# Kernel tuning notes

Hardware: AMD Instinct MI355X
Metric: run time of the kernel (lower is better)

Reference implementation:

```python
import jax, jax.numpy as jnp
import numpy as np

D_MODEL = 1024
N_HEADS = 16
D_FF = 4096
EPS = 1e-5


def setup_inputs() -> dict:
    key = jax.random.key(0)
    ks = jax.random.split(key, 16)
    B, S, D, F = 2, 2048, D_MODEL, D_FF
    s_d = 1.0 / np.sqrt(D)
    s_f = 1.0 / np.sqrt(F)
    return {
        "x": jax.random.normal(ks[0], (B, S, D), dtype=jnp.float32),
        "pad_mask": jnp.ones((B, S), dtype=jnp.int32),
        "ln1_g": jnp.ones((D,), jnp.float32), "ln1_b": jnp.zeros((D,), jnp.float32),
        "ln2_g": jnp.ones((D,), jnp.float32), "ln2_b": jnp.zeros((D,), jnp.float32),
        # weights stored [in, out] (equivalent to torch Linear weight.T)
        "wq": jax.random.normal(ks[1], (D, D), jnp.float32) * s_d,
        "bq": jnp.zeros((D,), jnp.float32),
        "wk": jax.random.normal(ks[2], (D, D), jnp.float32) * s_d,
        "bk": jnp.zeros((D,), jnp.float32),
        "wv": jax.random.normal(ks[3], (D, D), jnp.float32) * s_d,
        "bv": jnp.zeros((D,), jnp.float32),
        "wo": jax.random.normal(ks[4], (D, D), jnp.float32) * s_d,
        "bo": jnp.zeros((D,), jnp.float32),
        "w1": jax.random.normal(ks[5], (D, F), jnp.float32) * s_d,
        "b1": jnp.zeros((F,), jnp.float32),
        "w2": jax.random.normal(ks[6], (F, D), jnp.float32) * s_f,
        "b2": jnp.zeros((D,), jnp.float32),
    }


def _layernorm(x, g, b):
    mu = jnp.mean(x, axis=-1, keepdims=True)
    var = jnp.mean(jnp.square(x - mu), axis=-1, keepdims=True)
    return (x - mu) * jax.lax.rsqrt(var + EPS) * g + b


def reference(x, pad_mask, ln1_g, ln1_b, ln2_g, ln2_b,
              wq, bq, wk, bk, wv, bv, wo, bo, w1, b1, w2, b2):
    B, S, D = x.shape
    H = N_HEADS
    dk = D // H

    # mask: causal [1,1,S,S] * pad [B,1,1,S]
    causal = jnp.tril(jnp.ones((S, S), dtype=jnp.int32))[None, None]
    mask = pad_mask[:, None, None, :] * causal  # [B,1,S,S]

    h = _layernorm(x, ln1_g, ln1_b)
    q = (h @ wq + bq).reshape(B, S, H, dk).transpose(0, 2, 1, 3)
    k = (h @ wk + bk).reshape(B, S, H, dk).transpose(0, 2, 1, 3)
    v = (h @ wv + bv).reshape(B, S, H, dk).transpose(0, 2, 1, 3)

    scores = jnp.einsum('bhqd,bhkd->bhqk', q, k) / np.sqrt(dk)
    scores = jnp.where(mask == 0, -jnp.inf, scores)
    attn = jax.nn.softmax(scores, axis=-1)
    ctx = jnp.einsum('bhqk,bhkd->bhqd', attn, v)
    ctx = ctx.transpose(0, 2, 1, 3).reshape(B, S, D)
    x = x + ctx @ wo + bo

    h2 = _layernorm(x, ln2_g, ln2_b)
    ff = jax.nn.gelu(h2 @ w1 + b1, approximate=False) @ w2 + b2
    return x + ff
```

## Files before the change

kernel.cpp:

```cpp
#include <hip/hip_runtime.h>
#include <math.h>


typedef unsigned short bfu;
typedef unsigned short u16x4 __attribute__((ext_vector_type(4)));
typedef unsigned short u16x8 __attribute__((ext_vector_type(8)));
typedef __bf16         bf16x8 __attribute__((ext_vector_type(8)));
typedef float          f32x4 __attribute__((ext_vector_type(4)));

#define SEQ   2048
#define NTOK  4096
#define DM    1024
#define DKH   64

static __device__ __forceinline__ float bfu2f(bfu u) {
  return __uint_as_float(((unsigned)u) << 16);
}
static __device__ __forceinline__ bfu f2bfu(float f) {
  unsigned u = __float_as_uint(f);
  u += 0x7FFFu + ((u >> 16) & 1u);
  return (bfu)(u >> 16);
}
static __device__ __forceinline__ float ldF(const void* p, size_t i, bool isbf) {
  return isbf ? bfu2f(((const bfu*)p)[i]) : ((const float*)p)[i];
}
static __device__ __forceinline__ bool dt_isbf(const void* dt) {
  return *(const unsigned*)dt == 0x3F803F80u;
}
static __device__ __forceinline__ void g2l16(const void* g, void* l) {
  __builtin_amdgcn_global_load_lds((const __attribute__((address_space(1))) void*)g,
                                   (__attribute__((address_space(3))) void*)l,
                                   16, 0, 0);
}

static __device__ __forceinline__ void tr_tile(const void* in, bfu* out,
                                               int R, int C, int gx, int gy,
                                               bool isbf, bfu t[64][65]) {
  const int tx = threadIdx.x & 63, ty = threadIdx.x >> 6;
#pragma unroll
  for (int i = 0; i < 16; ++i) {
    int rr = i * 4 + ty;
    size_t idx = (size_t)(gy + rr) * C + gx + tx;
    t[rr][tx] = isbf ? ((const bfu*)in)[idx] : f2bfu(((const float*)in)[idx]);
  }
  __syncthreads();
#pragma unroll
  for (int i = 0; i < 16; ++i) {
    int cc = i * 4 + ty;
    out[(size_t)(gx + cc) * R + gy + tx] = t[tx][cc];
  }
}

__global__ __launch_bounds__(256) void prep_k(
    const void* ln1g, const void* ln1b, const void* ln2g, const void* ln2b,
    const void* bq, const void* bk, const void* bv, const void* bo,
    const void* b1, const void* b2,
    const void* wq, const void* wk, const void* wv, const void* wo,
    const void* w1, const void* w2,
    bfu* __restrict__ vecs, bfu* __restrict__ wqkvT, bfu* __restrict__ woT,
    bfu* __restrict__ w1T, bfu* __restrict__ w2T) {
  __shared__ bfu t[64][65];
  const bool isbf = dt_isbf(ln1g);
  const int bid = blockIdx.x, tid = threadIdx.x;
  if (bid < 52) {
    const void* src; int segStart, segDst;
    if      (bid < 4)  { src = ln1g; segStart = 0;  segDst = 0; }
    else if (bid < 8)  { src = ln1b; segStart = 4;  segDst = 1024; }
    else if (bid < 12) { src = ln2g; segStart = 8;  segDst = 2048; }
    else if (bid < 16) { src = ln2b; segStart = 12; segDst = 3072; }
    else if (bid < 20) { src = bq;   segStart = 16; segDst = 4096; }
    else if (bid < 24) { src = bk;   segStart = 20; segDst = 5120; }
    else if (bid < 28) { src = bv;   segStart = 24; segDst = 6144; }
    else if (bid < 32) { src = bo;   segStart = 28; segDst = 7168; }
    else if (bid < 48) { src = b1;   segStart = 32; segDst = 8192; }
    else               { src = b2;   segStart = 48; segDst = 12288; }
    const int off = (bid - segStart) * 256 + tid;
    vecs[segDst + off] = isbf ? ((const bfu*)src)[off]
                              : f2bfu(((const float*)src)[off]);
    return;
  }
  const void* in; bfu* out; int R, C, gx, gy;
  const int j = bid - 52;
  if (j < 1024) {
    const int mat = j >> 8, rem = j & 255;
    in  = (mat == 0) ? wq : (mat == 1) ? wk : (mat == 2) ? wv : wo;
    out = (mat == 0) ? wqkvT : (mat == 1) ? wqkvT + 1048576
        : (mat == 2) ? wqkvT + 2097152 : woT;
    R = 1024; C = 1024; gx = (rem & 15) * 64; gy = (rem >> 4) * 64;
  } else if (j < 2048) {
    const int rem = j - 1024;
    in = w1; out = w1T; R = 1024; C = 4096;
    gx = (rem & 63) * 64; gy = (rem >> 6) * 64;
  } else {
    const int rem = j - 2048;
    in = w2; out = w2T; R = 4096; C = 1024;
    gx = (rem & 15) * 64; gy = (rem >> 4) * 64;
  }
  tr_tile(in, out, R, C, gx, gy, isbf, t);
}

__global__ __launch_bounds__(256) void trw2_k(const void* __restrict__ w2,
                                              bfu* __restrict__ out,
                                              const void* __restrict__ dt) {
  __shared__ bfu t[64][65];
  const bool isbf = dt_isbf(dt);
  const int rem = blockIdx.x;
  tr_tile(w2, out, 4096, 1024, (rem & 15) * 64, (rem >> 4) * 64, isbf, t);
}

template <bool RAW>
__global__ __launch_bounds__(256) void ln_k(const void* __restrict__ xin,
                                            const bfu* __restrict__ g,
                                            const bfu* __restrict__ bb,
                                            bfu* __restrict__ y,
                                            const void* __restrict__ dt) {
  const int t = threadIdx.x;
  const size_t base = (size_t)blockIdx.x * DM;
  const int c0 = t * 4;
  float v[4];
  bool isbf = true;
  if constexpr (RAW) isbf = dt_isbf(dt);
  if (!RAW || isbf) {
    u16x4 u = *(const u16x4*)((const bfu*)xin + base + c0);
#pragma unroll
    for (int i = 0; i < 4; ++i) v[i] = bfu2f(u[i]);
  } else {
    float4 f = *(const float4*)((const float*)xin + base + c0);
    v[0] = f.x; v[1] = f.y; v[2] = f.z; v[3] = f.w;
  }
  float s1 = v[0] + v[1] + v[2] + v[3];
  float s2 = v[0]*v[0] + v[1]*v[1] + v[2]*v[2] + v[3]*v[3];
#pragma unroll
  for (int o = 32; o; o >>= 1) {
    s1 += __shfl_xor(s1, o);
    s2 += __shfl_xor(s2, o);
  }
  __shared__ float r1[4], r2[4];
  const int wid = t >> 6, lane = t & 63;
  if (lane == 0) { r1[wid] = s1; r2[wid] = s2; }
  __syncthreads();
  s1 = r1[0] + r1[1] + r1[2] + r1[3];
  s2 = r2[0] + r2[1] + r2[2] + r2[3];
  const float mu = s1 * (1.0f / DM);
  const float var = s2 * (1.0f / DM) - mu * mu;
  const float rs = rsqrtf(var + 1e-5f);
  u16x4 gv = *(const u16x4*)&g[c0];
  u16x4 bv = *(const u16x4*)&bb[c0];
  u16x4 ov;
#pragma unroll
  for (int i = 0; i < 4; ++i)
    ov[i] = f2bfu((v[i] - mu) * rs * bfu2f(gv[i]) + bfu2f(bv[i]));
  *(u16x4*)&y[base + c0] = ov;
}

template <int EPI, int BM>
__global__ __launch_bounds__(256) void gemm_bt(const bfu* __restrict__ A,
                                               const bfu* __restrict__ Bt,
                                               const bfu* __restrict__ bias,
                                               const void* __restrict__ res,
                                               void* __restrict__ C,
                                               int M, int N, int K,
                                               const void* __restrict__ dt) {
  constexpr int NF = (BM == 128) ? 4 : 2;
  __shared__ __align__(16) bfu Asm[BM * 32];
  __shared__ __align__(16) bfu Bsm[128 * 32];
  const bool isbf = dt_isbf(dt);
  const int tid = threadIdx.x;
  const int m0 = blockIdx.y * BM, n0 = blockIdx.x * 128;
  const int wid = tid >> 6, lane = tid & 63;
  const int wm = (BM == 128) ? (wid >> 1) * 64 : 0;
  const int wn = (BM == 128) ? (wid & 1) * 64 : wid * 32;
  const int quad = lane >> 4, l16 = lane & 15;

  f32x4 acc[4][NF] = {};

  const int c0 = tid, c1 = tid + 256;
  const bfu* agp0 = A + (size_t)(m0 + (c0 >> 2)) * K + (c0 & 3) * 8;
  const bfu* agp1 = A + (size_t)(m0 + ((c1 >> 2) & (BM - 1))) * K + (c1 & 3) * 8;
  const bfu* bgp0 = Bt + (size_t)(n0 + (c0 >> 2)) * K + (c0 & 3) * 8;
  const bfu* bgp1 = Bt + (size_t)(n0 + (c1 >> 2)) * K + (c1 & 3) * 8;
  bfu* al0 = Asm + c0 * 8;
  bfu* al1 = Asm + (BM == 128 ? c1 * 8 : 0);
  bfu* bl0 = Bsm + c0 * 8;
  bfu* bl1 = Bsm + c1 * 8;

  for (int k0 = 0; k0 < K; k0 += 32) {
    g2l16(agp0 + k0, al0);
    if constexpr (BM == 128) g2l16(agp1 + k0, al1);
    g2l16(bgp0 + k0, bl0);
    g2l16(bgp1 + k0, bl1);
    __syncthreads();

    u16x8 af[4], bfr[NF];
#pragma unroll
    for (int i = 0; i < 4; ++i)
      af[i] = *(const u16x8*)&Asm[(wm + i * 16 + l16) * 32 + quad * 8];
#pragma unroll
    for (int i = 0; i < NF; ++i)
      bfr[i] = *(const u16x8*)&Bsm[(wn + i * 16 + l16) * 32 + quad * 8];
#pragma unroll
    for (int mi = 0; mi < 4; ++mi)
#pragma unroll
      for (int ni = 0; ni < NF; ++ni)
        acc[mi][ni] = __builtin_amdgcn_mfma_f32_16x16x32_bf16(
            __builtin_bit_cast(bf16x8, af[mi]),
            __builtin_bit_cast(bf16x8, bfr[ni]), acc[mi][ni], 0, 0, 0);
    __syncthreads();
  }

#pragma unroll
  for (int mi = 0; mi < 4; ++mi) {
#pragma unroll
    for (int ni = 0; ni < NF; ++ni) {
      const int col = n0 + wn + ni * 16 + l16;
      const float bvv = bfu2f(bias[col]);
#pragma unroll
      for (int r = 0; r < 4; ++r) {
        const int row = m0 + wm + mi * 16 + quad * 4 + r;
        const size_t idx = (size_t)row * N + col;
        float v = acc[mi][ni][r] + bvv;
        if constexpr (EPI == 1) {
          v = 0.5f * v * (1.0f + erff(v * 0.70710678118f));
          ((bfu*)C)[idx] = f2bfu(v);
        } else if constexpr (EPI == 2) {
          v += ldF(res, idx, isbf);
          ((bfu*)C)[idx] = f2bfu(v);
        } else if constexpr (EPI == 3) {
          v += bfu2f(((const bfu*)res)[idx]);
          if (isbf) ((bfu*)C)[idx] = f2bfu(v);
          else      ((float*)C)[idx] = v;
        } else {
          ((bfu*)C)[idx] = f2bfu(v);
        }
      }
    }
  }
}

#define NEG_BIG (-1e30f)
#define KSTR 72

__global__ __launch_bounds__(256) void attn_flash(const bfu* __restrict__ qkv,
                                                  const int* __restrict__ pad,
                                                  bfu* __restrict__ ctx) {
  __shared__ __align__(16) bfu Kb[64 * KSTR];
  __shared__ __align__(16) bfu VT[64 * KSTR];
  __shared__ __align__(16) bfu Pb[4][16 * KSTR];

  const int tid = threadIdx.x;
  const int wid = tid >> 6, lane = tid & 63;
  const int quad = lane >> 4, l16 = lane & 15;
  const int bh = blockIdx.x;
  const int b = bh >> 4, h = bh & 15;
  const int yq = blockIdx.y;
  const int qt = (yq < 8) ? yq : (yq < 16) ? 23 - yq
               : (yq < 24) ? yq : 55 - yq;
  const int q0 = qt * 64;

  const bfu* qptr = qkv + (size_t)(b * SEQ + q0 + wid * 16 + l16) * 3072 + h * 64 + quad * 8;
  u16x8 qfr[2];
#pragma unroll
  for (int kt = 0; kt < 2; ++kt) {
    u16x8 qr = *(const u16x8*)(qptr + kt * 32);
#pragma unroll
    for (int j = 0; j < 8; ++j) qr[j] = f2bfu(bfu2f(qr[j]) * 0.125f);
    qfr[kt] = qr;
  }

  f32x4 Ofr[4] = {};
  float mrow[4], lrow[4];
#pragma unroll
  for (int r = 0; r < 4; ++r) { mrow[r] = NEG_BIG; lrow[r] = 0.0f; }

  const bfu* kvbase = qkv + (size_t)(b * SEQ) * 3072 + h * 64;
  const int* pb = pad + b * SEQ;
  const int qrow_base = q0 + wid * 16 + quad * 4;

  const int ntiles = qt + 1;
  for (int t = 0; t < ntiles; ++t) {
    const int k0 = t * 64;
    __syncthreads();

#pragma unroll
    for (int s = 0; s < 2; ++s) {
      const int cc = tid + s * 256;
      const int key = cc >> 3, pc = cc & 7;
      u16x8 kv8 = *(const u16x8*)(kvbase + (size_t)(k0 + key) * 3072 + 1024 + pc * 8);
      *(u16x8*)&Kb[key * KSTR + pc * 8] = kv8;
    }
    {
      const int vkey = tid & 63, dblk = tid >> 6;
      const bfu* vp = kvbase + (size_t)(k0 + vkey) * 3072 + 2048 + dblk * 16;
      u16x8 v0 = *(const u16x8*)vp;
      u16x8 v1 = *(const u16x8*)(vp + 8);
#pragma unroll
      for (int j = 0; j < 8; ++j) VT[(dblk * 16 + j) * KSTR + vkey] = v0[j];
#pragma unroll
      for (int j = 0; j < 8; ++j) VT[(dblk * 16 + 8 + j) * KSTR + vkey] = v1[j];
    }
    __syncthreads();

    f32x4 S[4] = {};
#pragma unroll
    for (int nt = 0; nt < 4; ++nt)
#pragma unroll
      for (int kt = 0; kt < 2; ++kt) {
        u16x8 bf = *(const u16x8*)&Kb[(nt * 16 + l16) * KSTR + kt * 32 + quad * 8];
        S[nt] = __builtin_amdgcn_mfma_f32_16x16x32_bf16(
            __builtin_bit_cast(bf16x8, qfr[kt]),
            __builtin_bit_cast(bf16x8, bf), S[nt], 0, 0, 0);
      }

    const bool edge = (t == qt);
    float p[4][4];
    float cmax[4] = {NEG_BIG, NEG_BIG, NEG_BIG, NEG_BIG};
#pragma unroll
    for (int nt = 0; nt < 4; ++nt) {
      const int key = k0 + nt * 16 + l16;
      const bool ok = (pb[key] != 0);
#pragma unroll
      for (int r = 0; r < 4; ++r) {
        float s = (ok && (!edge || key <= qrow_base + r)) ? S[nt][r] : NEG_BIG;
        p[nt][r] = s;
        cmax[r] = fmaxf(cmax[r], s);
      }
    }
#pragma unroll
    for (int off = 1; off < 16; off <<= 1)
#pragma unroll
      for (int r = 0; r < 4; ++r)
        cmax[r] = fmaxf(cmax[r], __shfl_xor(cmax[r], off));
    float alpha[4];
#pragma unroll
    for (int r = 0; r < 4; ++r) {
      const float mn = fmaxf(mrow[r], cmax[r]);
      alpha[r] = __expf(mrow[r] - mn);
      mrow[r] = mn;
    }
    float psum[4] = {0, 0, 0, 0};
#pragma unroll
    for (int nt = 0; nt < 4; ++nt)
#pragma unroll
      for (int r = 0; r < 4; ++r) {
        p[nt][r] = __expf(p[nt][r] - mrow[r]);
        psum[r] += p[nt][r];
      }
#pragma unroll
    for (int off = 1; off < 16; off <<= 1)
#pragma unroll
      for (int r = 0; r < 4; ++r) psum[r] += __shfl_xor(psum[r], off);
#pragma unroll
    for (int r = 0; r < 4; ++r) lrow[r] = lrow[r] * alpha[r] + psum[r];
#pragma unroll
    for (int n = 0; n < 4; ++n)
#pragma unroll
      for (int r = 0; r < 4; ++r) Ofr[n][r] *= alpha[r];

#pragma unroll
    for (int nt = 0; nt < 4; ++nt)
#pragma unroll
      for (int r = 0; r < 4; ++r)
        Pb[wid][(quad * 4 + r) * KSTR + nt * 16 + l16] = f2bfu(p[nt][r]);

#pragma unroll
    for (int at = 0; at < 2; ++at) {
      u16x8 af = *(const u16x8*)&Pb[wid][l16 * KSTR + at * 32 + quad * 8];
#pragma unroll
      for (int n = 0; n < 4; ++n) {
        u16x8 bf = *(const u16x8*)&VT[(n * 16 + l16) * KSTR + at * 32 + quad * 8];
        Ofr[n] = __builtin_amdgcn_mfma_f32_16x16x32_bf16(
            __builtin_bit_cast(bf16x8, af),
            __builtin_bit_cast(bf16x8, bf), Ofr[n], 0, 0, 0);
      }
    }
  }

  float inv[4];
#pragma unroll
  for (int r = 0; r < 4; ++r) inv[r] = 1.0f / lrow[r];
#pragma unroll
  for (int n = 0; n < 4; ++n)
#pragma unroll
    for (int r = 0; r < 4; ++r)
      ctx[(size_t)(b * SEQ + qrow_base + r) * DM + h * 64 + n * 16 + l16] =
          f2bfu(Ofr[n][r] * inv[r]);
}

extern "C" void kernel_launch(void* const* d_in, const int* in_sizes, int n_in,
                              void* d_out, int out_size, void* d_ws, size_t ws_size,
                              hipStream_t stream) {
  (void)in_sizes; (void)n_in; (void)out_size;
  const void* x    = d_in[0];
  const int*  pad  = (const int*)d_in[1];
  const void* ln1g = d_in[2];
  const void* ln1b = d_in[3];
  const void* ln2g = d_in[4];
  const void* ln2b = d_in[5];
  const void* wq   = d_in[6];
  const void* bq   = d_in[7];
  const void* wk   = d_in[8];
  const void* bk   = d_in[9];
  const void* wv   = d_in[10];
  const void* bv   = d_in[11];
  const void* wo   = d_in[12];
  const void* bo   = d_in[13];
  const void* w1   = d_in[14];
  const void* b1   = d_in[15];
  const void* w2   = d_in[16];
  const void* b2   = d_in[17];

  const bool flat = ws_size >= (size_t)(37765120 + 1024) * 2;
  bfu* base  = (bfu*)d_ws;
  bfu* vecs  = base;
  bfu* wqkvT = vecs  + 16384;
  bfu* woT   = wqkvT + 3145728;
  bfu* w1T   = woT   + 1048576;
  bfu* w2Tf  = w1T   + 4194304;
  bfu* h     = w2Tf  + (flat ? 4194304 : 0);
  bfu* qkv   = h     + 4194304;
  bfu* ctx   = qkv   + 12582912;
  bfu* x1    = ctx   + 4194304;
  bfu* ffh   = qkv;
  bfu* w2T   = flat ? w2Tf : h;

  const dim3 blk(256);
  bfu* lg1 = vecs;        bfu* lb1 = vecs + 1024;
  bfu* lg2 = vecs + 2048; bfu* lb2 = vecs + 3072;
  bfu* bqkv = vecs + 4096;
  bfu* boc  = vecs + 7168;
  bfu* b1c  = vecs + 8192;
  bfu* b2c  = vecs + 12288;

  prep_k<<<dim3(flat ? 3124 : 2100), blk, 0, stream>>>(
      ln1g, ln1b, ln2g, ln2b, bq, bk, bv, bo, b1, b2,
      wq, wk, wv, wo, w1, w2, vecs, wqkvT, woT, w1T, w2T);

  ln_k<true><<<dim3(NTOK), blk, 0, stream>>>(x, lg1, lb1, h, ln1g);
  gemm_bt<0, 128><<<dim3(24, 32), blk, 0, stream>>>(h, wqkvT, bqkv, nullptr,
                                                    qkv, NTOK, 3072, 1024, ln1g);
  attn_flash<<<dim3(32, 32), blk, 0, stream>>>(qkv, pad, ctx);
  gemm_bt<2, 64><<<dim3(8, 64), blk, 0, stream>>>(ctx, woT, boc, x, x1,
                                                  NTOK, 1024, 1024, ln1g);
  ln_k<false><<<dim3(NTOK), blk, 0, stream>>>(x1, lg2, lb2, h, ln1g);
  gemm_bt<1, 128><<<dim3(32, 32), blk, 0, stream>>>(h, w1T, b1c, nullptr, ffh,
                                                    NTOK, 4096, 1024, ln1g);
  if (!flat) trw2_k<<<dim3(1024), blk, 0, stream>>>(w2, w2T, ln1g);
  gemm_bt<3, 64><<<dim3(8, 64), blk, 0, stream>>>(ffh, w2T, b2c, x1, d_out,
                                                  NTOK, 1024, 4096, ln1g);
}
```

Before: 472.0 us.

## Add 32-row GEMM tile variant for N=1024 GEMMs and prefetch K/V tiles in attention

Result: faster. 452.4 us (-4.2%).

```diff
diff --git a/kernel.cpp b/kernel.cpp
--- a/kernel.cpp
+++ b/kernel.cpp
@@ -153,7 +153,7 @@
   *(u16x4*)&y[base + c0] = ov;
 }
 
-template <int EPI, int BM>
+template <int EPI>
 __global__ __launch_bounds__(256) void gemm_bt(const bfu* __restrict__ A,
                                                const bfu* __restrict__ Bt,
                                                const bfu* __restrict__ bias,
@@ -161,47 +161,45 @@
                                                void* __restrict__ C,
                                                int M, int N, int K,
                                                const void* __restrict__ dt) {
-  constexpr int NF = (BM == 128) ? 4 : 2;
-  __shared__ __align__(16) bfu Asm[BM * 32];
+  __shared__ __align__(16) bfu Asm[128 * 32];
   __shared__ __align__(16) bfu Bsm[128 * 32];
   const bool isbf = dt_isbf(dt);
   const int tid = threadIdx.x;
-  const int m0 = blockIdx.y * BM, n0 = blockIdx.x * 128;
+  const int m0 = blockIdx.y * 128, n0 = blockIdx.x * 128;
   const int wid = tid >> 6, lane = tid & 63;
-  const int wm = (BM == 128) ? (wid >> 1) * 64 : 0;
-  const int wn = (BM == 128) ? (wid & 1) * 64 : wid * 32;
+  const int wm = (wid >> 1) * 64, wn = (wid & 1) * 64;
   const int quad = lane >> 4, l16 = lane & 15;
 
-  f32x4 acc[4][NF] = {};
+  f32x4 acc[4][4] = {};
 
   const int c0 = tid, c1 = tid + 256;
   const bfu* agp0 = A + (size_t)(m0 + (c0 >> 2)) * K + (c0 & 3) * 8;
-  const bfu* agp1 = A + (size_t)(m0 + ((c1 >> 2) & (BM - 1))) * K + (c1 & 3) * 8;
+  const bfu* agp1 = A + (size_t)(m0 + (c1 >> 2)) * K + (c1 & 3) * 8;
   const bfu* bgp0 = Bt + (size_t)(n0 + (c0 >> 2)) * K + (c0 & 3) * 8;
   const bfu* bgp1 = Bt + (size_t)(n0 + (c1 >> 2)) * K + (c1 & 3) * 8;
   bfu* al0 = Asm + c0 * 8;
-  bfu* al1 = Asm + (BM == 128 ? c1 * 8 : 0);
+  bfu* al1 = Asm + c1 * 8;
   bfu* bl0 = Bsm + c0 * 8;
   bfu* bl1 = Bsm + c1 * 8;
 
   for (int k0 = 0; k0 < K; k0 += 32) {
     g2l16(agp0 + k0, al0);
-    if constexpr (BM == 128) g2l16(agp1 + k0, al1);
+    g2l16(agp1 + k0, al1);
     g2l16(bgp0 + k0, bl0);
     g2l16(bgp1 + k0, bl1);
     __syncthreads();
 
-    u16x8 af[4], bfr[NF];
+    u16x8 af[4], bfr[4];
 #pragma unroll
     for (int i = 0; i < 4; ++i)
       af[i] = *(const u16x8*)&Asm[(wm + i * 16 + l16) * 32 + quad * 8];
 #pragma unroll
-    for (int i = 0; i < NF; ++i)
+    for (int i = 0; i < 4; ++i)
       bfr[i] = *(const u16x8*)&Bsm[(wn + i * 16 + l16) * 32 + quad * 8];
 #pragma unroll
     for (int mi = 0; mi < 4; ++mi)
 #pragma unroll
-      for (int ni = 0; ni < NF; ++ni)
+      for (int ni = 0; ni < 4; ++ni)
         acc[mi][ni] = __builtin_amdgcn_mfma_f32_16x16x32_bf16(
             __builtin_bit_cast(bf16x8, af[mi]),
             __builtin_bit_cast(bf16x8, bfr[ni]), acc[mi][ni], 0, 0, 0);
@@ -211,7 +209,7 @@
 #pragma unroll
   for (int mi = 0; mi < 4; ++mi) {
 #pragma unroll
-    for (int ni = 0; ni < NF; ++ni) {
+    for (int ni = 0; ni < 4; ++ni) {
       const int col = n0 + wn + ni * 16 + l16;
       const float bvv = bfu2f(bias[col]);
 #pragma unroll
@@ -237,6 +235,94 @@
   }
 }
 
+template <int EPI>
+__global__ __launch_bounds__(256) void gemm32_bt(const bfu* __restrict__ A,
+                                                 const bfu* __restrict__ Bt,
+                                                 const bfu* __restrict__ bias,
+                                                 const void* __restrict__ res,
+                                                 void* __restrict__ C,
+                                                 int M, int N, int K,
+                                                 const void* __restrict__ dt) {
+  __shared__ __align__(16) bfu Asm[2 * 32 * 32];
+  __shared__ __align__(16) bfu Bsm[2 * 128 * 32];
+  const bool isbf = dt_isbf(dt);
+  const int tid = threadIdx.x;
+  const int m0 = blockIdx.y * 32, n0 = blockIdx.x * 128;
+  const int wid = tid >> 6, lane = tid & 63;
+  const int wn = wid * 32;
+  const int quad = lane >> 4, l16 = lane & 15;
+
+  f32x4 acc[2][2] = {};
+
+  const int pA = tid >> 7, rA = (tid >> 2) & 31, qA = tid & 3;
+  const bfu* agp = A + (size_t)(m0 + rA) * K + pA * 32 + qA * 8;
+  bfu* aldst = Asm + tid * 8;
+  const bfu* bgp[4]; bfu* bldst[4];
+#pragma unroll
+  for (int s = 0; s < 4; ++s) {
+    const int c = tid + s * 256;
+    const int pB = c >> 9, rB = (c >> 2) & 127, qB = c & 3;
+    bgp[s] = Bt + (size_t)(n0 + rB) * K + pB * 32 + qB * 8;
+    bldst[s] = Bsm + c * 8;
+  }
+
+  for (int k0 = 0; k0 < K; k0 += 64) {
+    g2l16(agp + k0, aldst);
+#pragma unroll
+    for (int s = 0; s < 4; ++s) g2l16(bgp[s] + k0, bldst[s]);
+    __syncthreads();
+
+    u16x8 af[2][2], bfr[2][2];
+#pragma unroll
+    for (int kt = 0; kt < 2; ++kt) {
+#pragma unroll
+      for (int mi = 0; mi < 2; ++mi)
+        af[mi][kt] = *(const u16x8*)&Asm[kt * 1024 + (mi * 16 + l16) * 32 + quad * 8];
+#pragma unroll
+      for (int ni = 0; ni < 2; ++ni)
+        bfr[ni][kt] = *(const u16x8*)&Bsm[kt * 4096 + (wn + ni * 16 + l16) * 32 + quad * 8];
+    }
+#pragma unroll
+    for (int kt = 0; kt < 2; ++kt)
+#pragma unroll
+      for (int mi = 0; mi < 2; ++mi)
+#pragma unroll
+        for (int ni = 0; ni < 2; ++ni)
+          acc[mi][ni] = __builtin_amdgcn_mfma_f32_16x16x32_bf16(
+              __builtin_bit_cast(bf16x8, af[mi][kt]),
+              __builtin_bit_cast(bf16x8, bfr[ni][kt]), acc[mi][ni], 0, 0, 0);
+    __syncthreads();
+  }
+
+#pragma unroll
+  for (int mi = 0; mi < 2; ++mi) {
+#pragma unroll
+    for (int ni = 0; ni < 2; ++ni) {
+      const int col = n0 + wn + ni * 16 + l16;
+      const float bvv = bfu2f(bias[col]);
+#pragma unroll
+      for (int r = 0; r < 4; ++r) {
+        const int row = m0 + mi * 16 + quad * 4 + r;
+        const size_t idx = (size_t)row * N + col;
+        float v = acc[mi][ni][r] + bvv;
+        if constexpr (EPI == 1) {
+          v = 0.5f * v * (1.0f + erff(v * 0.70710678118f));
+          ((bfu*)C)[idx] = f2bfu(v);
+        } else if constexpr (EPI == 2) {
+          v += ldF(res, idx, isbf);
+          ((bfu*)C)[idx] = f2bfu(v);
+        } else if constexpr (EPI == 3) {
+          v += bfu2f(((const bfu*)res)[idx]);
+          if (isbf) ((bfu*)C)[idx] = f2bfu(v);
+          else      ((float*)C)[idx] = v;
+        } else {
+          ((bfu*)C)[idx] = f2bfu(v);
+        }
+      }
+    }
+  }
+}
+
 #define NEG_BIG (-1e30f)
 #define KSTR 72
 
@@ -276,29 +362,36 @@
   const int* pb = pad + b * SEQ;
   const int qrow_base = q0 + wid * 16 + quad * 4;
 
+  const int kkey0 = tid >> 3,          kpc0 = tid & 7;
+  const int kkey1 = (tid + 256) >> 3,  kpc1 = (tid + 256) & 7;
+  const int vkey = tid & 63, dblk = tid >> 6;
+
+  u16x8 kreg0, kreg1, vreg0, vreg1;
+  kreg0 = *(const u16x8*)(kvbase + (size_t)kkey0 * 3072 + 1024 + kpc0 * 8);
+  kreg1 = *(const u16x8*)(kvbase + (size_t)kkey1 * 3072 + 1024 + kpc1 * 8);
+  vreg0 = *(const u16x8*)(kvbase + (size_t)vkey * 3072 + 2048 + dblk * 16);
+  vreg1 = *(const u16x8*)(kvbase + (size_t)vkey * 3072 + 2048 + dblk * 16 + 8);
+
   const int ntiles = qt + 1;
   for (int t = 0; t < ntiles; ++t) {
     const int k0 = t * 64;
     __syncthreads();
 
-#pragma unroll
-    for (int s = 0; s < 2; ++s) {
-      const int cc = tid + s * 256;
-      const int key = cc >> 3, pc = cc & 7;
-      u16x8 kv8 = *(const u16x8*)(kvbase + (size_t)(k0 + key) * 3072 + 1024 + pc * 8);
-      *(u16x8*)&Kb[key * KSTR + pc * 8] = kv8;
-    }
-    {
-      const int vkey = tid & 63, dblk = tid >> 6;
-      const bfu* vp = kvbase + (size_t)(k0 + vkey) * 3072 + 2048 + dblk * 16;
-      u16x8 v0 = *(const u16x8*)vp;
-      u16x8 v1 = *(const u16x8*)(vp + 8);
-#pragma unroll
-      for (int j = 0; j < 8; ++j) VT[(dblk * 16 + j) * KSTR + vkey] = v0[j];
-#pragma unroll
-      for (int j = 0; j < 8; ++j) VT[(dblk * 16 + 8 + j) * KSTR + vkey] = v1[j];
-    }
+    *(u16x8*)&Kb[kkey0 * KSTR + kpc0 * 8] = kreg0;
+    *(u16x8*)&Kb[kkey1 * KSTR + kpc1 * 8] = kreg1;
+#pragma unroll
+    for (int j = 0; j < 8; ++j) VT[(dblk * 16 + j) * KSTR + vkey] = vreg0[j];
+#pragma unroll
+    for (int j = 0; j < 8; ++j) VT[(dblk * 16 + 8 + j) * KSTR + vkey] = vreg1[j];
     __syncthreads();
+
+    if (t + 1 < ntiles) {
+      const int kn = k0 + 64;
+      kreg0 = *(const u16x8*)(kvbase + (size_t)(kn + kkey0) * 3072 + 1024 + kpc0 * 8);
+      kreg1 = *(const u16x8*)(kvbase + (size_t)(kn + kkey1) * 3072 + 1024 + kpc1 * 8);
+      vreg0 = *(const u16x8*)(kvbase + (size_t)(kn + vkey) * 3072 + 2048 + dblk * 16);
+      vreg1 = *(const u16x8*)(kvbase + (size_t)(kn + vkey) * 3072 + 2048 + dblk * 16 + 8);
+    }
 
     f32x4 S[4] = {};
 #pragma unroll
@@ -436,15 +529,15 @@
       wq, wk, wv, wo, w1, w2, vecs, wqkvT, woT, w1T, w2T);
 
   ln_k<true><<<dim3(NTOK), blk, 0, stream>>>(x, lg1, lb1, h, ln1g);
-  gemm_bt<0, 128><<<dim3(24, 32), blk, 0, stream>>>(h, wqkvT, bqkv, nullptr,
-                                                    qkv, NTOK, 3072, 1024, ln1g);
+  gemm_bt<0><<<dim3(24, 32), blk, 0, stream>>>(h, wqkvT, bqkv, nullptr,
+                                               qkv, NTOK, 3072, 1024, ln1g);
   attn_flash<<<dim3(32, 32), blk, 0, stream>>>(qkv, pad, ctx);
-  gemm_bt<2, 64><<<dim3(8, 64), blk, 0, stream>>>(ctx, woT, boc, x, x1,
-                                                  NTOK, 1024, 1024, ln1g);
+  gemm32_bt<2><<<dim3(8, 128), blk, 0, stream>>>(ctx, woT, boc, x, x1,
+                                                 NTOK, 1024, 1024, ln1g);
   ln_k<false><<<dim3(NTOK), blk, 0, stream>>>(x1, lg2, lb2, h, ln1g);
-  gemm_bt<1, 128><<<dim3(32, 32), blk, 0, stream>>>(h, w1T, b1c, nullptr, ffh,
-                                                    NTOK, 4096, 1024, ln1g);
+  gemm_bt<1><<<dim3(32, 32), blk, 0, stream>>>(h, w1T, b1c, nullptr, ffh,
+                                               NTOK, 4096, 1024, ln1g);
   if (!flat) trw2_k<<<dim3(1024), blk, 0, stream>>>(w2, w2T, ln1g);
-  gemm_bt<3, 64><<<dim3(8, 64), blk, 0, stream>>>(ffh, w2T, b2c, x1, d_out,
-                                                  NTOK, 1024, 4096, ln1g);
-}
+  gemm32_bt<3><<<dim3(8, 128), blk, 0, stream>>>(ffh, w2T, b2c, x1, d_out,
+                                                 NTOK, 1024, 4096, ln1g);
+}
```
